# Kernel tuning notes

Hardware: AMD Instinct MI355X
Metric: run time of the kernel (lower is better)

## Reference

```python
import jax, jax.numpy as jnp
import numpy as np

INPUT_SIZE = 512
HIDDEN_SIZE = 512
BATCH = 64
SEQ_LEN = 512


def _xavier(key, shape):
    fan_in, fan_out = shape[0], shape[1]
    limit = float(np.sqrt(6.0 / (fan_in + fan_out)))
    return jax.random.uniform(key, shape, jnp.float32, -limit, limit)


def setup_inputs() -> dict:
    key = jax.random.key(0)
    ks = jax.random.split(key, 14)
    inp = {
        "inputs": jax.random.normal(ks[0], (BATCH, SEQ_LEN, INPUT_SIZE), jnp.float32),
        "W_i": _xavier(ks[1], (INPUT_SIZE, HIDDEN_SIZE)),
        "W_f": _xavier(ks[2], (INPUT_SIZE, HIDDEN_SIZE)),
        "W_o": _xavier(ks[3], (INPUT_SIZE, HIDDEN_SIZE)),
        "W_c": _xavier(ks[4], (INPUT_SIZE, HIDDEN_SIZE)),
        "U_i": _xavier(ks[5], (HIDDEN_SIZE, HIDDEN_SIZE)),
        "U_f": _xavier(ks[6], (HIDDEN_SIZE, HIDDEN_SIZE)),
        "U_o": _xavier(ks[7], (HIDDEN_SIZE, HIDDEN_SIZE)),
        "U_c": _xavier(ks[8], (HIDDEN_SIZE, HIDDEN_SIZE)),
        "b_i": _xavier(ks[9], (1, HIDDEN_SIZE)),
        "b_f": _xavier(ks[10], (1, HIDDEN_SIZE)),
        "b_o": _xavier(ks[11], (1, HIDDEN_SIZE)),
        "b_c": _xavier(ks[12], (1, HIDDEN_SIZE)),
    }
    return inp


def reference(inputs, W_i, W_f, W_o, W_c, U_i, U_f, U_o, U_c, b_i, b_f, b_o, b_c):
    B, S, D = inputs.shape
    H = W_i.shape[1]
    # Fuse the 4 input projections into one GEMM over the whole sequence
    # (same math as per-step separate matmuls, just batched).
    W = jnp.concatenate([W_i, W_f, W_o, W_c], axis=1)      # [D, 4H]
    U = jnp.concatenate([U_i, U_f, U_o, U_c], axis=1)      # [H, 4H]
    b = jnp.concatenate([b_i, b_f, b_o, b_c], axis=1)      # [1, 4H]
    x_proj = jnp.einsum('bsd,dg->sbg', inputs, W) + b      # [S, B, 4H]

    def step(carry, xp):
        h, c = carry
        gates = xp + h @ U                                  # [B, 4H]
        i_g = jax.nn.sigmoid(gates[:, 0*H:1*H])
        f_g = jax.nn.sigmoid(gates[:, 1*H:2*H])
        o_g = jax.nn.sigmoid(gates[:, 2*H:3*H])
        c_t = jnp.tanh(gates[:, 3*H:4*H])
        c_new = f_g * c + i_g * c_t
        h_new = o_g * jnp.tanh(c_new)
        return (h_new, c_new), None

    h0 = jnp.zeros((B, H), jnp.float32)
    c0 = jnp.zeros((B, H), jnp.float32)
    (h_final, _), _ = jax.lax.scan(step, (h0, c0), x_proj)
    return h_final
```

## Files before the change

### kernel.cpp

```cpp
#include <hip/hip_runtime.h>


#define NG   4
#define GR   16
#define NS   32
#define SC   16
#define DIM  512
#define HID  512
#define SEQ  512
#define NTHR 256
#define NWG  (NG*NS)

#define AOFF 0
#define GOFF (GR*1024)
#define BOFF (GOFF + 4096)
#define LDS_BYTES (BOFF + 64*2048)

#define WS_FLAG_BYTES 16384
#define HBUF_UINTS   (2*NG*GR*256)
#define WS_NEED      (WS_FLAG_BYTES + HBUF_UINTS*4)

typedef float f32x4  __attribute__((ext_vector_type(4)));
typedef short bf16x8 __attribute__((ext_vector_type(8)));

union HPack { unsigned u[4]; bf16x8 v; };

__device__ __forceinline__ unsigned short f2bf(float f){
  union { float f; unsigned u; } v; v.f = f;
  unsigned r = v.u + 0x7fffu + ((v.u >> 16) & 1u);
  return (unsigned short)(r >> 16);
}
__device__ __forceinline__ float sigm(float x){ return 1.0f/(1.0f + __expf(-x)); }
__device__ __forceinline__ float tanh_f(float x){
  float e = __expf(-2.0f * fabsf(x));
  float t = (1.0f - e)/(1.0f + e);
  return x < 0.0f ? -t : t;
}

__global__ void zero_ws_kernel(uint4* p, int n4){
  int i = blockIdx.x*blockDim.x + threadIdx.x;
  uint4 z; z.x=0u; z.y=0u; z.z=0u; z.w=0u;
  if (i < n4) p[i] = z;
}

__global__ __launch_bounds__(NTHR, 1) void lstm_persistent(
  const float* __restrict__ x,
  const float* __restrict__ W0, const float* __restrict__ W1,
  const float* __restrict__ W2, const float* __restrict__ W3,
  const float* __restrict__ U0, const float* __restrict__ U1,
  const float* __restrict__ U2, const float* __restrict__ U3,
  const float* __restrict__ b0, const float* __restrict__ b1,
  const float* __restrict__ b2, const float* __restrict__ b3,
  float* __restrict__ out,
  unsigned* __restrict__ flags,
  unsigned* __restrict__ hbuf32)
{
  __shared__ __align__(16) char smem[LDS_BYTES];
  const int tid = threadIdx.x;
  const int bid = blockIdx.x;
  const int g = bid >> 5;
  const int s = bid & 31;
  const int w = tid >> 6;
  const int l = tid & 63;

  {
    const int q  = tid & 3;
    const int kk = tid >> 2;
    for (int gate = 0; gate < 4; ++gate){
      const float* Wsrc = (gate==0)?W0:(gate==1)?W1:(gate==2)?W2:W3;
      const float* Usrc = (gate==0)?U0:(gate==1)?U1:(gate==2)?U2:U3;
      #pragma unroll
      for (int kb = 0; kb < 16; ++kb){
        const int k = kb*64 + kk;
        const float* p = (k < DIM)
          ? (Wsrc + (size_t)k*HID + s*SC + q*4)
          : (Usrc + (size_t)(k-DIM)*HID + s*SC + q*4);
        f32x4 v = *(const f32x4*)p;
        #pragma unroll
        for (int j = 0; j < 4; ++j){
          const int c = gate*16 + q*4 + j;
          const unsigned byte = ((unsigned)(k*2)) ^ ((unsigned)((c&7)<<4));
          *(unsigned short*)(&smem[BOFF + c*2048] + byte) = f2bf(v[j]);
        }
      }
    }
  }

  const int er = tid >> 4;
  const int ec = tid & 15;
  const int ecol = s*SC + ec;
  const float bi = b0[ecol], bff = b1[ecol], bo = b2[ecol], bc = b3[ecol];
  float cstate = 0.0f, hout = 0.0f;

  const int arow = l & 15;
  const int qh   = l >> 4;
  const unsigned swz = (unsigned)((arow & 7) << 4);
  const char* Abase = &smem[AOFF + arow*1024];
  const char* Bbase = &smem[BOFF + (w*16 + arow)*2048];
  float* gatesLds = (float*)&smem[GOFF];

  const int sr  = tid >> 4;
  const int sdb = tid & 15;
  const unsigned swzS = (unsigned)((sr & 7) << 4);
  char* Arow = &smem[AOFF + sr*1024];

  unsigned* gflags = flags + g*1024;
  const float* xrow = x + (size_t)(g*GR + sr)*SEQ*DIM + sdb*32;
  const unsigned* hrow_base = hbuf32 + (size_t)(g*GR + sr)*256 + sdb*16;

  f32x4 xr[8];
  HPack hp[4];

#define GEMM_STEP(QA, QB, ACC) do { \
    bf16x8 a_ = *(const bf16x8*)(Abase + (((unsigned)((QA)*64 + qh*16)) ^ swz)); \
    bf16x8 b_ = *(const bf16x8*)(Bbase + (((unsigned)((QB)*64 + qh*16)) ^ swz)); \
    ACC = __builtin_amdgcn_mfma_f32_16x16x32_bf16(a_, b_, ACC, 0, 0, 0); \
  } while(0)

  {
    const float* xp = xrow;
    #pragma unroll
    for (int j = 0; j < 8; ++j) xr[j] = *(const f32x4*)(xp + j*4);
  }

  __syncthreads();

  for (int t = 0; t < SEQ; ++t){
    if (t > 0 && tid < 32){
      const unsigned* fp = &gflags[tid*32];
      while (__hip_atomic_load(fp, __ATOMIC_RELAXED, __HIP_MEMORY_SCOPE_AGENT)
             < (unsigned)t) { }
    }
    __syncthreads();

    if (t > 0){
      const unsigned* hsrc = hrow_base + (size_t)((t&1)*NG)*GR*256;
      #pragma unroll
      for (int j = 0; j < 4; ++j){
        #pragma unroll
        for (int e = 0; e < 4; ++e)
          hp[j].u[e] = __hip_atomic_load(hsrc + j*4 + e, __ATOMIC_RELAXED,
                                         __HIP_MEMORY_SCOPE_AGENT);
      }
    }

    #pragma unroll
    for (int j = 0; j < 4; ++j){
      f32x4 u = xr[2*j], v = xr[2*j+1];
      bf16x8 o8;
      o8[0]=(short)f2bf(u[0]); o8[1]=(short)f2bf(u[1]);
      o8[2]=(short)f2bf(u[2]); o8[3]=(short)f2bf(u[3]);
      o8[4]=(short)f2bf(v[0]); o8[5]=(short)f2bf(v[1]);
      o8[6]=(short)f2bf(v[2]); o8[7]=(short)f2bf(v[3]);
      *(bf16x8*)(Arow + (((unsigned)(sdb*64 + j*16)) ^ swzS)) = o8;
    }
    __syncthreads();

    f32x4 acc0 = {0.f,0.f,0.f,0.f}, acc1 = {0.f,0.f,0.f,0.f};
    f32x4 acc2 = {0.f,0.f,0.f,0.f}, acc3 = {0.f,0.f,0.f,0.f};

    #pragma unroll
    for (int q4 = 0; q4 < 4; ++q4){
      GEMM_STEP(q4*4+0, q4*4+0, acc0);
      GEMM_STEP(q4*4+1, q4*4+1, acc1);
      GEMM_STEP(q4*4+2, q4*4+2, acc2);
      GEMM_STEP(q4*4+3, q4*4+3, acc3);
    }
    __syncthreads();

    if (t > 0){
      #pragma unroll
      for (int j = 0; j < 4; ++j)
        *(bf16x8*)(Arow + (((unsigned)(sdb*64 + j*16)) ^ swzS)) = hp[j].v;
    }
    __syncthreads();

    if (t > 0){
      #pragma unroll
      for (int q4 = 0; q4 < 4; ++q4){
        GEMM_STEP(q4*4+0, q4*4+16, acc0);
        GEMM_STEP(q4*4+1, q4*4+17, acc1);
        GEMM_STEP(q4*4+2, q4*4+18, acc2);
        GEMM_STEP(q4*4+3, q4*4+19, acc3);
      }
    }

    f32x4 accs = (acc0 + acc1) + (acc2 + acc3);
    #pragma unroll
    for (int rr = 0; rr < 4; ++rr)
      gatesLds[(qh*4 + rr)*64 + w*16 + arow] = accs[rr];
    __syncthreads();

    {
      float gi = gatesLds[er*64 +  0 + ec] + bi;
      float gf = gatesLds[er*64 + 16 + ec] + bff;
      float go = gatesLds[er*64 + 32 + ec] + bo;
      float gc = gatesLds[er*64 + 48 + ec] + bc;
      float ig = sigm(gi), fg = sigm(gf), og = sigm(go), ct = tanh_f(gc);
      cstate = fg*cstate + ig*ct;
      hout = og * tanh_f(cstate);
      unsigned hb = (unsigned)f2bf(hout);
      unsigned ob = __shfl_xor(hb, 1);
      if ((tid & 1) == 0){
        unsigned val = hb | (ob << 16);
        unsigned idx = (unsigned)((((t+1)&1)*NG + g)*GR + er)*256u
                     + (unsigned)(s*8 + (ec>>1));
        __hip_atomic_store(hbuf32 + idx, val, __ATOMIC_RELAXED,
                           __HIP_MEMORY_SCOPE_AGENT);
      }
    }
    __syncthreads();

    {
      const int tn = (t + 1 < SEQ) ? (t + 1) : t;
      const float* xp = xrow + (size_t)tn*DIM;
      #pragma unroll
      for (int j = 0; j < 8; ++j) xr[j] = *(const f32x4*)(xp + j*4);
    }

    if (tid == 0)
      __hip_atomic_store(&gflags[s*32], (unsigned)(t+1),
                         __ATOMIC_RELAXED, __HIP_MEMORY_SCOPE_AGENT);
  }

  out[(size_t)(g*GR + er)*HID + s*SC + ec] = hout;
#undef GEMM_STEP
}

extern "C" void kernel_launch(void* const* d_in, const int* in_sizes, int n_in,
                              void* d_out, int out_size, void* d_ws, size_t ws_size,
                              hipStream_t stream)
{
  (void)in_sizes; (void)n_in; (void)out_size;
  if (ws_size < (size_t)WS_NEED) return;

  const float* x  = (const float*)d_in[0];
  const float* W0 = (const float*)d_in[1];
  const float* W1 = (const float*)d_in[2];
  const float* W2 = (const float*)d_in[3];
  const float* W3 = (const float*)d_in[4];
  const float* U0 = (const float*)d_in[5];
  const float* U1 = (const float*)d_in[6];
  const float* U2 = (const float*)d_in[7];
  const float* U3 = (const float*)d_in[8];
  const float* b0 = (const float*)d_in[9];
  const float* b1 = (const float*)d_in[10];
  const float* b2 = (const float*)d_in[11];
  const float* b3 = (const float*)d_in[12];
  float* out = (float*)d_out;

  unsigned* flags  = (unsigned*)d_ws;
  unsigned* hbuf32 = (unsigned*)((char*)d_ws + WS_FLAG_BYTES);

  const int n4 = WS_NEED / 16;
  zero_ws_kernel<<<dim3((n4 + 255)/256), dim3(256), 0, stream>>>((uint4*)d_ws, n4);
  lstm_persistent<<<dim3(NWG), dim3(NTHR), 0, stream>>>(
      x, W0,W1,W2,W3, U0,U1,U2,U3, b0,b1,b2,b3, out, flags, hbuf32);
}
```

Before: 2.977 ms.

## Replace per-block flags with step-tagged h words and overlap h fetch with input GEMM

Each hidden-state word now carries the timestep number in its upper 32 bits, so consumers poll the data itself instead of waiting on per-block flags followed by a separate load. The h loads are issued before the input-projection MFMAs so their latency overlaps the GEMM. The next x prefetch is moved earlier, and __syncthreads is replaced by an lgkmcnt wait plus s_barrier. This removes the flag round trip and two barriers per step, at the cost of doubling h-buffer traffic and relying on 64-bit atomic stores being seen whole.

```diff
diff --git a/kernel.cpp b/kernel.cpp
--- a/kernel.cpp
+++ b/kernel.cpp
@@ -16,14 +16,16 @@
 #define BOFF (GOFF + 4096)
 #define LDS_BYTES (BOFF + 64*2048)
 
-#define WS_FLAG_BYTES 16384
-#define HBUF_UINTS   (2*NG*GR*256)
-#define WS_NEED      (WS_FLAG_BYTES + HBUF_UINTS*4)
+#define HBUF_WORDS (2*NG*GR*256)
+#define WS_NEED    (HBUF_WORDS*8)
 
 typedef float f32x4  __attribute__((ext_vector_type(4)));
 typedef short bf16x8 __attribute__((ext_vector_type(8)));
-
-union HPack { unsigned u[4]; bf16x8 v; };
+typedef unsigned long long u64;
+
+union Pk { unsigned u[4]; bf16x8 v; };
+
+#define BARRIER() asm volatile("s_waitcnt lgkmcnt(0)\n\ts_barrier" ::: "memory")
 
 __device__ __forceinline__ unsigned short f2bf(float f){
   union { float f; unsigned u; } v; v.f = f;
@@ -52,8 +54,7 @@
   const float* __restrict__ b0, const float* __restrict__ b1,
   const float* __restrict__ b2, const float* __restrict__ b3,
   float* __restrict__ out,
-  unsigned* __restrict__ flags,
-  unsigned* __restrict__ hbuf32)
+  u64* __restrict__ hbuf)
 {
   __shared__ __align__(16) char smem[LDS_BYTES];
   const int tid = threadIdx.x;
@@ -104,12 +105,13 @@
   const unsigned swzS = (unsigned)((sr & 7) << 4);
   char* Arow = &smem[AOFF + sr*1024];
 
-  unsigned* gflags = flags + g*1024;
   const float* xrow = x + (size_t)(g*GR + sr)*SEQ*DIM + sdb*32;
-  const unsigned* hrow_base = hbuf32 + (size_t)(g*GR + sr)*256 + sdb*16;
+  const u64* hsrc0 = hbuf + ((size_t)g*GR + sr)*256 + sdb*16;
+  const u64* hsrc1 = hbuf + ((size_t)(NG + g)*GR + sr)*256 + sdb*16;
+  const size_t pidx = ((size_t)g*GR + er)*256 + (size_t)(s*8 + (ec>>1));
 
   f32x4 xr[8];
-  HPack hp[4];
+  u64   hp[16];
 
 #define GEMM_STEP(QA, QB, ACC) do { \
     bf16x8 a_ = *(const bf16x8*)(Abase + (((unsigned)((QA)*64 + qh*16)) ^ swz)); \
@@ -117,33 +119,12 @@
     ACC = __builtin_amdgcn_mfma_f32_16x16x32_bf16(a_, b_, ACC, 0, 0, 0); \
   } while(0)
 
-  {
-    const float* xp = xrow;
-    #pragma unroll
-    for (int j = 0; j < 8; ++j) xr[j] = *(const f32x4*)(xp + j*4);
-  }
+  #pragma unroll
+  for (int j = 0; j < 8; ++j) xr[j] = *(const f32x4*)(xrow + j*4);
 
   __syncthreads();
 
   for (int t = 0; t < SEQ; ++t){
-    if (t > 0 && tid < 32){
-      const unsigned* fp = &gflags[tid*32];
-      while (__hip_atomic_load(fp, __ATOMIC_RELAXED, __HIP_MEMORY_SCOPE_AGENT)
-             < (unsigned)t) { }
-    }
-    __syncthreads();
-
-    if (t > 0){
-      const unsigned* hsrc = hrow_base + (size_t)((t&1)*NG)*GR*256;
-      #pragma unroll
-      for (int j = 0; j < 4; ++j){
-        #pragma unroll
-        for (int e = 0; e < 4; ++e)
-          hp[j].u[e] = __hip_atomic_load(hsrc + j*4 + e, __ATOMIC_RELAXED,
-                                         __HIP_MEMORY_SCOPE_AGENT);
-      }
-    }
-
     #pragma unroll
     for (int j = 0; j < 4; ++j){
       f32x4 u = xr[2*j], v = xr[2*j+1];
@@ -154,7 +135,15 @@
       o8[6]=(short)f2bf(v[2]); o8[7]=(short)f2bf(v[3]);
       *(bf16x8*)(Arow + (((unsigned)(sdb*64 + j*16)) ^ swzS)) = o8;
     }
-    __syncthreads();
+    BARRIER();
+
+    const u64* hsrc = (t & 1) ? hsrc1 : hsrc0;
+    if (t > 0){
+      #pragma unroll
+      for (int j = 0; j < 16; ++j)
+        hp[j] = __hip_atomic_load(hsrc + j, __ATOMIC_RELAXED,
+                                  __HIP_MEMORY_SCOPE_AGENT);
+    }
 
     f32x4 acc0 = {0.f,0.f,0.f,0.f}, acc1 = {0.f,0.f,0.f,0.f};
     f32x4 acc2 = {0.f,0.f,0.f,0.f}, acc3 = {0.f,0.f,0.f,0.f};
@@ -166,14 +155,34 @@
       GEMM_STEP(q4*4+2, q4*4+2, acc2);
       GEMM_STEP(q4*4+3, q4*4+3, acc3);
     }
-    __syncthreads();
+    BARRIER();
 
     if (t > 0){
-      #pragma unroll
-      for (int j = 0; j < 4; ++j)
-        *(bf16x8*)(Arow + (((unsigned)(sdb*64 + j*16)) ^ swzS)) = hp[j].v;
-    }
-    __syncthreads();
+      const unsigned want = (unsigned)t;
+      unsigned pend = 0xffffu;
+      while (pend){
+        unsigned np = 0u;
+        #pragma unroll
+        for (int j = 0; j < 16; ++j){
+          if (pend & (1u << j)){
+            if ((unsigned)(hp[j] >> 32) != want){
+              hp[j] = __hip_atomic_load(hsrc + j, __ATOMIC_RELAXED,
+                                        __HIP_MEMORY_SCOPE_AGENT);
+              if ((unsigned)(hp[j] >> 32) != want) np |= (1u << j);
+            }
+          }
+        }
+        pend = np;
+      }
+      #pragma unroll
+      for (int q = 0; q < 4; ++q){
+        Pk pk;
+        #pragma unroll
+        for (int e = 0; e < 4; ++e) pk.u[e] = (unsigned)hp[q*4 + e];
+        *(bf16x8*)(Arow + (((unsigned)(sdb*64 + q*16)) ^ swzS)) = pk.v;
+      }
+    }
+    BARRIER();
 
     if (t > 0){
       #pragma unroll
@@ -185,11 +194,18 @@
       }
     }
 
+    {
+      const int tn = (t + 1 < SEQ) ? (t + 1) : t;
+      const float* xp = xrow + (size_t)tn*DIM;
+      #pragma unroll
+      for (int j = 0; j < 8; ++j) xr[j] = *(const f32x4*)(xp + j*4);
+    }
+
     f32x4 accs = (acc0 + acc1) + (acc2 + acc3);
     #pragma unroll
     for (int rr = 0; rr < 4; ++rr)
       gatesLds[(qh*4 + rr)*64 + w*16 + arow] = accs[rr];
-    __syncthreads();
+    BARRIER();
 
     {
       float gi = gatesLds[er*64 +  0 + ec] + bi;
@@ -202,25 +218,13 @@
       unsigned hb = (unsigned)f2bf(hout);
       unsigned ob = __shfl_xor(hb, 1);
       if ((tid & 1) == 0){
-        unsigned val = hb | (ob << 16);
-        unsigned idx = (unsigned)((((t+1)&1)*NG + g)*GR + er)*256u
-                     + (unsigned)(s*8 + (ec>>1));
-        __hip_atomic_store(hbuf32 + idx, val, __ATOMIC_RELAXED,
+        u64 val = ((u64)(unsigned)(t + 1) << 32)
+                | (u64)(hb | (ob << 16));
+        u64* dst = hbuf + (size_t)(((t+1)&1)*NG)*GR*256 + pidx;
+        __hip_atomic_store(dst, val, __ATOMIC_RELAXED,
                            __HIP_MEMORY_SCOPE_AGENT);
       }
     }
-    __syncthreads();
-
-    {
-      const int tn = (t + 1 < SEQ) ? (t + 1) : t;
-      const float* xp = xrow + (size_t)tn*DIM;
-      #pragma unroll
-      for (int j = 0; j < 8; ++j) xr[j] = *(const f32x4*)(xp + j*4);
-    }
-
-    if (tid == 0)
-      __hip_atomic_store(&gflags[s*32], (unsigned)(t+1),
-                         __ATOMIC_RELAXED, __HIP_MEMORY_SCOPE_AGENT);
   }
 
   out[(size_t)(g*GR + er)*HID + s*SC + ec] = hout;
@@ -249,11 +253,10 @@
   const float* b3 = (const float*)d_in[12];
   float* out = (float*)d_out;
 
-  unsigned* flags  = (unsigned*)d_ws;
-  unsigned* hbuf32 = (unsigned*)((char*)d_ws + WS_FLAG_BYTES);
+  u64* hbuf = (u64*)d_ws;
 
   const int n4 = WS_NEED / 16;
   zero_ws_kernel<<<dim3((n4 + 255)/256), dim3(256), 0, stream>>>((uint4*)d_ws, n4);
   lstm_persistent<<<dim3(NWG), dim3(NTHR), 0, stream>>>(
-      x, W0,W1,W2,W3, U0,U1,U2,U3, b0,b1,b2,b3, out, flags, hbuf32);
-}
+      x, W0,W1,W2,W3, U0,U1,U2,U3, b0,b1,b2,b3, out, hbuf);
+}
```

Result: faster. 2.589 ms (-13.0%).
